# Kernel optimization log

Measured on AMD Instinct MI355X. Metric: run time of the kernel, lower is better.

The kernel has to match this reference:

```python
import jax, jax.numpy as jnp
import numpy as np

B, S, D, H = 2, 2048, 1024, 8
DK = D // H            # 128
TOPK = int(0.25 * S)   # 512, matches int(topk_ratio * attn_scores.shape[-1])


def setup_inputs() -> dict:
    root = jax.random.key(0)
    ks = jax.random.split(root, 11)
    s = 1.0 / np.sqrt(D)  # nn.Linear default init scale
    def lin(kw, kb):
        W = jax.random.uniform(kw, (D, D), jnp.float32, -s, s)
        b = jax.random.uniform(kb, (D,), jnp.float32, -s, s)
        return W, b
    Wq, bq = lin(ks[0], ks[1])
    Wk, bk = lin(ks[2], ks[3])
    Wv, bv = lin(ks[4], ks[5])
    Wo, bo = lin(ks[6], ks[7])
    return {
        "query": jax.random.normal(ks[8], (B, S, D), jnp.float32),
        "key": jax.random.normal(ks[9], (B, S, D), jnp.float32),
        "value": jax.random.normal(ks[10], (B, S, D), jnp.float32),
        "Wq": Wq, "bq": bq, "Wk": Wk, "bk": bk,
        "Wv": Wv, "bv": bv, "Wo": Wo, "bo": bo,
    }


def reference(query, key, value, Wq, bq, Wk, bk, Wv, bv, Wo, bo):
    # Projections + split heads: [B,S,D] -> [B,S,H,DK]
    Q = (query @ Wq + bq).reshape(B, S, H, DK)
    K = (key   @ Wk + bk).reshape(B, S, H, DK)
    V = (value @ Wv + bv).reshape(B, S, H, DK)

    # Full attention scores [B,H,S,S]
    scores = jnp.einsum('nqhd,nkhd->nhqk', Q, K) / np.sqrt(DK).astype(np.float32)

    # Top-k per query row, scatter into a -1e20-filled tensor
    top_val, top_idx = jax.lax.top_k(scores, TOPK)  # [B,H,S,TOPK]
    bi = jnp.arange(B)[:, None, None, None]
    hi = jnp.arange(H)[None, :, None, None]
    qi = jnp.arange(S)[None, None, :, None]
    sparse = jnp.full(scores.shape, -1e20, scores.dtype).at[bi, hi, qi, top_idx].set(top_val)

    weights = jax.nn.softmax(sparse, axis=-1)                      # [B,H,S,S]
    attn = jnp.einsum('nhql,nlhd->nqhd', weights, V).reshape(B, S, D)
    out = attn @ Wo + bo
    return out, weights
```

## Files before the change

### kernel.cpp

```cpp
#include <hip/hip_runtime.h>
#include <hip/hip_bf16.h>
#include <math.h>

namespace {

constexpr int Bb   = 2;
constexpr int Ss   = 2048;
constexpr int Dd   = 1024;
constexpr int Hh   = 8;
constexpr int DKk  = 128;
constexpr int KTOP = 512;
constexpr int BH    = Bb * Hh;
constexpr int MROWS = Bb * Ss;
constexpr float SCALE = 0.08838834764831845f;

typedef __attribute__((ext_vector_type(8))) short short8t;
typedef __attribute__((ext_vector_type(4))) short short4t;
typedef __attribute__((ext_vector_type(4))) float f32x4;

__device__ inline ushort f2bf(float x) {
  const unsigned u = __float_as_uint(x);
  return (ushort)((u + 0x7FFFu + ((u >> 16) & 1u)) >> 16);
}
__device__ inline float bf2f(ushort h) {
  return __uint_as_float(((unsigned)h) << 16);
}
struct HL { short h, l; };
__device__ inline HL split1(float x) {
  HL r;
  const ushort hu = f2bf(x);
  r.h = (short)hu;
  r.l = (short)f2bf(x - bf2f(hu));
  return r;
}

__device__ inline unsigned key_of(float v) {
  const unsigned u = __float_as_uint(v);
  return (u & 0x80000000u) ? ~u : (u | 0x80000000u);
}
__device__ inline float key_to_float(unsigned k) {
  const unsigned u = (k & 0x80000000u) ? (k & 0x7FFFFFFFu) : ~k;
  return __uint_as_float(u);
}

__device__ inline void gload16(const void* g, void* l) {
  __builtin_amdgcn_global_load_lds(
      (const __attribute__((address_space(1))) unsigned int*)g,
      (__attribute__((address_space(3))) unsigned int*)l, 16, 0, 0);
}

__global__ __launch_bounds__(256) void split_inputs(
    const float* __restrict__ query, const float* __restrict__ keyi,
    const float* __restrict__ value,
    ushort* __restrict__ qsh, ushort* __restrict__ qsl,
    ushort* __restrict__ ksh, ushort* __restrict__ ksl,
    ushort* __restrict__ vsb)
{
  const int z = blockIdx.y;
  const size_t i = ((size_t)blockIdx.x * 256 + threadIdx.x) * 8;
  const float* src = (z == 0) ? query : (z == 1) ? keyi : value;
  const float4 v0 = *(const float4*)(src + i);
  const float4 v1 = *(const float4*)(src + i + 4);
  if (z < 2) {
    ushort* oh = (z == 0) ? qsh : ksh;
    ushort* ol = (z == 0) ? qsl : ksl;
    short8t h, lo;
    HL r;
    r = split1(v0.x); h[0] = r.h; lo[0] = r.l;
    r = split1(v0.y); h[1] = r.h; lo[1] = r.l;
    r = split1(v0.z); h[2] = r.h; lo[2] = r.l;
    r = split1(v0.w); h[3] = r.h; lo[3] = r.l;
    r = split1(v1.x); h[4] = r.h; lo[4] = r.l;
    r = split1(v1.y); h[5] = r.h; lo[5] = r.l;
    r = split1(v1.z); h[6] = r.h; lo[6] = r.l;
    r = split1(v1.w); h[7] = r.h; lo[7] = r.l;
    *(short8t*)(oh + i) = h;
    *(short8t*)(ol + i) = lo;
  } else {
    short8t h;
    h[0] = (short)f2bf(v0.x); h[1] = (short)f2bf(v0.y);
    h[2] = (short)f2bf(v0.z); h[3] = (short)f2bf(v0.w);
    h[4] = (short)f2bf(v1.x); h[5] = (short)f2bf(v1.y);
    h[6] = (short)f2bf(v1.z); h[7] = (short)f2bf(v1.w);
    *(short8t*)(vsb + i) = h;
  }
}

__global__ __launch_bounds__(256) void transpose_prep(
    const float* __restrict__ Wq, const float* __restrict__ Wk,
    const float* __restrict__ Wv, const float* __restrict__ Wo,
    ushort* __restrict__ WqTh, ushort* __restrict__ WqTl,
    ushort* __restrict__ WkTh, ushort* __restrict__ WkTl,
    ushort* __restrict__ WvT,  ushort* __restrict__ WoT)
{
  __shared__ float tile[32][33];
  const int z = blockIdx.z;
  const float* W = (z == 0) ? Wq : (z == 1) ? Wk : (z == 2) ? Wv : Wo;
  const int t  = threadIdx.x;
  const int c0 = blockIdx.x * 32, r0 = blockIdx.y * 32;
  const int lr = t >> 3, lc4 = (t & 7) * 4;
  const float4 v = *(const float4*)(W + (size_t)(r0 + lr) * Dd + c0 + lc4);
  tile[lr][lc4 + 0] = v.x; tile[lr][lc4 + 1] = v.y;
  tile[lr][lc4 + 2] = v.z; tile[lr][lc4 + 3] = v.w;
  __syncthreads();
  const int oc = t >> 3, or4 = (t & 7) * 4;
  const size_t o = (size_t)(c0 + oc) * Dd + r0 + or4;
  if (z < 2) {
    ushort* Th = (z == 0) ? WqTh : WkTh;
    ushort* Tl = (z == 0) ? WqTl : WkTl;
    short4t oh, ol;
    HL r;
    r = split1(tile[or4 + 0][oc]); oh[0] = r.h; ol[0] = r.l;
    r = split1(tile[or4 + 1][oc]); oh[1] = r.h; ol[1] = r.l;
    r = split1(tile[or4 + 2][oc]); oh[2] = r.h; ol[2] = r.l;
    r = split1(tile[or4 + 3][oc]); oh[3] = r.h; ol[3] = r.l;
    *(short4t*)(Th + o) = oh;
    *(short4t*)(Tl + o) = ol;
  } else {
    ushort* Wt = (z == 2) ? WvT : WoT;
    short4t ov;
    ov[0] = (short)f2bf(tile[or4 + 0][oc]);
    ov[1] = (short)f2bf(tile[or4 + 1][oc]);
    ov[2] = (short)f2bf(tile[or4 + 2][oc]);
    ov[3] = (short)f2bf(tile[or4 + 3][oc]);
    *(short4t*)(Wt + o) = ov;
  }
}

__global__ __launch_bounds__(256) void mfma_proj(
    const ushort* __restrict__ qsh, const ushort* __restrict__ qsl,
    const ushort* __restrict__ ksh, const ushort* __restrict__ ksl,
    const ushort* __restrict__ vsb,
    const ushort* __restrict__ WqTh, const ushort* __restrict__ WqTl,
    const ushort* __restrict__ WkTh, const ushort* __restrict__ WkTl,
    const ushort* __restrict__ WvT,
    const float* __restrict__ bq, const float* __restrict__ bk,
    const float* __restrict__ bv,
    ushort* __restrict__ Qh, ushort* __restrict__ Ql,
    ushort* __restrict__ Kh, ushort* __restrict__ Kl,
    ushort* __restrict__ Vt)
{
  __shared__ ushort Ah[128 * 32];
  __shared__ ushort Al[128 * 32];
  __shared__ ushort Bh[128 * 32];
  __shared__ ushort Bl[128 * 32];
  const int t  = threadIdx.x;
  const int z  = blockIdx.z;
  const int m0 = blockIdx.x * 128;
  const int n0 = blockIdx.y * 128;
  const int l  = t & 63, wv = t >> 6;
  const int wr = wv >> 1, wc = wv & 1;
  const int lrow = l & 15, lhi = l >> 4;

  const ushort* Ah_g = (z == 0) ? qsh : (z == 1) ? ksh : vsb;
  const ushort* Al_g = (z == 0) ? qsl : (z == 1) ? ksl : nullptr;
  const ushort* Bth  = (z == 0) ? WqTh : (z == 1) ? WkTh : WvT;
  const ushort* Btl  = (z == 0) ? WqTl : (z == 1) ? WkTl : nullptr;
  const float*  bias = (z == 0) ? bq   : (z == 1) ? bk   : bv;
  const bool    splitTerms = (z < 2);

  f32x4 acc[4][4] = {};

  for (int kt = 0; kt < Dd; kt += 32) {
#pragma unroll
    for (int p = 0; p < 2; ++p) {
      const int baseRow = p * 64 + wv * 16;
      const int row  = baseRow + (l >> 2);
      const int gl   = (l & 3) ^ (row & 3);
      const size_t ao = (size_t)(m0 + row) * Dd + kt + gl * 8;
      const size_t bo = (size_t)(n0 + row) * Dd + kt + gl * 8;
      gload16(Ah_g + ao, &Ah[baseRow * 32]);
      gload16(Bth + bo, &Bh[baseRow * 32]);
      if (splitTerms) {
        gload16(Al_g + ao, &Al[baseRow * 32]);
        gload16(Btl + bo, &Bl[baseRow * 32]);
      }
    }
    __syncthreads();

    short8t ah[4], al[4], bh[4], bl[4];
#pragma unroll
    for (int i = 0; i < 4; ++i) {
      const int row = wr * 64 + i * 16 + lrow;
      const int idx = row * 32 + ((lhi ^ (row & 3)) << 3);
      ah[i] = *(const short8t*)&Ah[idx];
      if (splitTerms) al[i] = *(const short8t*)&Al[idx];
    }
#pragma unroll
    for (int j = 0; j < 4; ++j) {
      const int row = wc * 64 + j * 16 + lrow;
      const int idx = row * 32 + ((lhi ^ (row & 3)) << 3);
      bh[j] = *(const short8t*)&Bh[idx];
      if (splitTerms) bl[j] = *(const short8t*)&Bl[idx];
    }
#pragma unroll
    for (int i = 0; i < 4; ++i)
#pragma unroll
      for (int j = 0; j < 4; ++j) {
        acc[i][j] = __builtin_amdgcn_mfma_f32_16x16x32_bf16(ah[i], bh[j], acc[i][j], 0, 0, 0);
        if (splitTerms) {
          acc[i][j] = __builtin_amdgcn_mfma_f32_16x16x32_bf16(ah[i], bl[j], acc[i][j], 0, 0, 0);
          acc[i][j] = __builtin_amdgcn_mfma_f32_16x16x32_bf16(al[i], bh[j], acc[i][j], 0, 0, 0);
        }
      }
    __syncthreads();
  }

#pragma unroll
  for (int i = 0; i < 4; ++i) {
#pragma unroll
    for (int j = 0; j < 4; ++j) {
      const int nn = n0 + wc * 64 + j * 16 + lrow;
#pragma unroll
      for (int r = 0; r < 4; ++r) {
        const int mm = m0 + wr * 64 + i * 16 + lhi * 4 + r;
        const float v = acc[i][j][r] + bias[nn];
        const int bb = mm >> 11, s = mm & (Ss - 1);
        const int hh = nn >> 7,  dk = nn & (DKk - 1);
        if (z < 2) {
          const size_t o = (((size_t)(bb * Hh + hh)) * Ss + s) * DKk + dk;
          const HL rr = split1(v);
          if (z == 0) { Qh[o] = (ushort)rr.h; Ql[o] = (ushort)rr.l; }
          else        { Kh[o] = (ushort)rr.h; Kl[o] = (ushort)rr.l; }
        } else {
          Vt[((size_t)((bb * Hh + hh) * DKk + dk)) * Ss + s] = f2bf(v);
        }
      }
    }
  }
}

__global__ __launch_bounds__(256) void mfma_scores(
    const ushort* __restrict__ Qh, const ushort* __restrict__ Ql,
    const ushort* __restrict__ Kh, const ushort* __restrict__ Kl,
    unsigned* __restrict__ wtsOut)
{
  __shared__ ushort Ah[128 * 32];
  __shared__ ushort Al[128 * 32];
  __shared__ ushort Bh[128 * 32];
  __shared__ ushort Bl[128 * 32];
  const int t  = threadIdx.x;
  const int z  = blockIdx.z;
  const int n0 = blockIdx.x * 128;
  const int m0 = blockIdx.y * 128;
  const int l  = t & 63, wv = t >> 6;
  const int wr = wv >> 1, wc = wv & 1;
  const int lrow = l & 15, lhi = l >> 4;
  const size_t boff = (size_t)z * Ss * DKk;

  f32x4 acc[4][4] = {};

  for (int kt = 0; kt < DKk; kt += 32) {
#pragma unroll
    for (int p = 0; p < 2; ++p) {
      const int baseRow = p * 64 + wv * 16;
      const int row  = baseRow + (l >> 2);
      const int gl   = (l & 3) ^ (row & 3);
      const size_t ao = boff + (size_t)(m0 + row) * DKk + kt + gl * 8;
      const size_t bo = boff + (size_t)(n0 + row) * DKk + kt + gl * 8;
      gload16(Qh + ao, &Ah[baseRow * 32]);
      gload16(Ql + ao, &Al[baseRow * 32]);
      gload16(Kh + bo, &Bh[baseRow * 32]);
      gload16(Kl + bo, &Bl[baseRow * 32]);
    }
    __syncthreads();

    short8t ah[4], al[4], bh[4], bl[4];
#pragma unroll
    for (int i = 0; i < 4; ++i) {
      const int row = wr * 64 + i * 16 + lrow;
      const int idx = row * 32 + ((lhi ^ (row & 3)) << 3);
      ah[i] = *(const short8t*)&Ah[idx];
      al[i] = *(const short8t*)&Al[idx];
    }
#pragma unroll
    for (int j = 0; j < 4; ++j) {
      const int row = wc * 64 + j * 16 + lrow;
      const int idx = row * 32 + ((lhi ^ (row & 3)) << 3);
      bh[j] = *(const short8t*)&Bh[idx];
      bl[j] = *(const short8t*)&Bl[idx];
    }
#pragma unroll
    for (int i = 0; i < 4; ++i)
#pragma unroll
      for (int j = 0; j < 4; ++j) {
        acc[i][j] = __builtin_amdgcn_mfma_f32_16x16x32_bf16(ah[i], bh[j], acc[i][j], 0, 0, 0);
        acc[i][j] = __builtin_amdgcn_mfma_f32_16x16x32_bf16(ah[i], bl[j], acc[i][j], 0, 0, 0);
        acc[i][j] = __builtin_amdgcn_mfma_f32_16x16x32_bf16(al[i], bh[j], acc[i][j], 0, 0, 0);
      }
    __syncthreads();
  }

#pragma unroll
  for (int i = 0; i < 4; ++i)
#pragma unroll
    for (int j = 0; j < 4; ++j) {
      const int nn = n0 + wc * 64 + j * 16 + lrow;
#pragma unroll
      for (int r = 0; r < 4; ++r) {
        const int mm = m0 + wr * 64 + i * 16 + lhi * 4 + r;
        wtsOut[(size_t)z * Ss * Ss + (size_t)mm * Ss + nn] =
            key_of(acc[i][j][r] * SCALE);
      }
    }
}

__global__ __launch_bounds__(256) void mfma_oproj(
    const float* __restrict__ pv0, const float* __restrict__ pv1,
    const ushort* __restrict__ Bt,
    const float* __restrict__ bias, float* __restrict__ Cout)
{
  __shared__ ushort As[128 * 64];
  __shared__ ushort Bs[128 * 64];
  const int t  = threadIdx.x;
  const int m0 = blockIdx.x * 128;
  const int n0 = blockIdx.y * 128;
  const int l  = t & 63, wv = t >> 6;
  const int wr = wv >> 1, wc = wv & 1;
  const int lrow = l & 15, lhi = l >> 4;

  f32x4 acc[4][4] = {};

  for (int kt = 0; kt < Dd; kt += 64) {
#pragma unroll
    for (int p = 0; p < 4; ++p) {
      const int baseRow = p * 32 + wv * 8;
      const int brow = baseRow + (l >> 3);
      const int bgl  = (l & 7) ^ (brow & 7);
      gload16(Bt + (size_t)(n0 + brow) * Dd + kt + bgl * 8, &Bs[baseRow * 64]);
      const int li = p * 256 + t, row = li >> 3, g = li & 7;
      const int sw = row * 64 + ((g ^ (row & 7)) << 3);
      const size_t ao = (size_t)(m0 + row) * Dd + kt + g * 8;
      const float4 a0 = *(const float4*)(pv0 + ao);
      const float4 a1 = *(const float4*)(pv0 + ao + 4);
      const float4 c0 = *(const float4*)(pv1 + ao);
      const float4 c1 = *(const float4*)(pv1 + ao + 4);
      short8t sa;
      sa[0] = (short)f2bf(a0.x + c0.x); sa[1] = (short)f2bf(a0.y + c0.y);
      sa[2] = (short)f2bf(a0.z + c0.z); sa[3] = (short)f2bf(a0.w + c0.w);
      sa[4] = (short)f2bf(a1.x + c1.x); sa[5] = (short)f2bf(a1.y + c1.y);
      sa[6] = (short)f2bf(a1.z + c1.z); sa[7] = (short)f2bf(a1.w + c1.w);
      *(short8t*)&As[sw] = sa;
    }
    __syncthreads();

#pragma unroll
    for (int kk = 0; kk < 2; ++kk) {
      short8t a[4], b[4];
      const int g = kk * 4 + lhi;
#pragma unroll
      for (int i = 0; i < 4; ++i) {
        const int row = wr * 64 + i * 16 + lrow;
        a[i] = *(const short8t*)&As[row * 64 + ((g ^ (row & 7)) << 3)];
      }
#pragma unroll
      for (int j = 0; j < 4; ++j) {
        const int row = wc * 64 + j * 16 + lrow;
        b[j] = *(const short8t*)&Bs[row * 64 + ((g ^ (row & 7)) << 3)];
      }
#pragma unroll
      for (int i = 0; i < 4; ++i)
#pragma unroll
        for (int j = 0; j < 4; ++j)
          acc[i][j] = __builtin_amdgcn_mfma_f32_16x16x32_bf16(a[i], b[j], acc[i][j], 0, 0, 0);
    }
    __syncthreads();
  }

#pragma unroll
  for (int i = 0; i < 4; ++i)
#pragma unroll
    for (int j = 0; j < 4; ++j) {
      const int nn = n0 + wc * 64 + j * 16 + lrow;
#pragma unroll
      for (int r = 0; r < 4; ++r) {
        const int mm = m0 + wr * 64 + i * 16 + lhi * 4 + r;
        Cout[(size_t)mm * Dd + nn] = acc[i][j][r] + bias[nn];
      }
    }
}

__global__ __launch_bounds__(256) void pv_split(
    const float* __restrict__ Wts, const ushort* __restrict__ VtAll,
    float* __restrict__ pvp)
{
  __shared__ ushort As[128 * 64];
  __shared__ ushort Bs[128 * 64];
  const int t  = threadIdx.x;
  const int ks = blockIdx.x;
  const int m0 = blockIdx.y * 128;
  const int z  = blockIdx.z;
  const int l  = t & 63, wv = t >> 6;
  const int wr = wv >> 1, wc = wv & 1;
  const int lrow = l & 15, lhi = l >> 4;

  const float*  Af = Wts + (size_t)z * Ss * Ss;
  const ushort* Bt = VtAll + (size_t)z * DKk * Ss;

  f32x4 acc[4][4] = {};

  for (int kt = ks * 1024; kt < ks * 1024 + 1024; kt += 64) {
#pragma unroll
    for (int p = 0; p < 4; ++p) {
      const int baseRow = p * 32 + wv * 8;
      const int brow = baseRow + (l >> 3);
      const int bgl  = (l & 7) ^ (brow & 7);
      gload16(Bt + (size_t)brow * Ss + kt + bgl * 8, &Bs[baseRow * 64]);
      const int li = p * 256 + t, row = li >> 3, g = li & 7;
      const int sw = row * 64 + ((g ^ (row & 7)) << 3);
      const float* src = Af + (size_t)(m0 + row) * Ss + kt + g * 8;
      const float4 v0 = *(const float4*)src;
      const float4 v1 = *(const float4*)(src + 4);
      short8t sa;
      sa[0] = (short)f2bf(v0.x); sa[1] = (short)f2bf(v0.y);
      sa[2] = (short)f2bf(v0.z); sa[3] = (short)f2bf(v0.w);
      sa[4] = (short)f2bf(v1.x); sa[5] = (short)f2bf(v1.y);
      sa[6] = (short)f2bf(v1.z); sa[7] = (short)f2bf(v1.w);
      *(short8t*)&As[sw] = sa;
    }
    __syncthreads();

#pragma unroll
    for (int kk = 0; kk < 2; ++kk) {
      short8t a[4], b[4];
      const int g = kk * 4 + lhi;
#pragma unroll
      for (int i = 0; i < 4; ++i) {
        const int row = wr * 64 + i * 16 + lrow;
        a[i] = *(const short8t*)&As[row * 64 + ((g ^ (row & 7)) << 3)];
      }
#pragma unroll
      for (int j = 0; j < 4; ++j) {
        const int row = wc * 64 + j * 16 + lrow;
        b[j] = *(const short8t*)&Bs[row * 64 + ((g ^ (row & 7)) << 3)];
      }
#pragma unroll
      for (int i = 0; i < 4; ++i)
#pragma unroll
        for (int j = 0; j < 4; ++j)
          acc[i][j] = __builtin_amdgcn_mfma_f32_16x16x32_bf16(a[i], b[j], acc[i][j], 0, 0, 0);
    }
    __syncthreads();
  }

  const int bb = z >> 3, hh = z & 7;
  float* outp = pvp + (size_t)ks * MROWS * Dd;
#pragma unroll
  for (int i = 0; i < 4; ++i)
#pragma unroll
    for (int j = 0; j < 4; ++j) {
      const int nn = wc * 64 + j * 16 + lrow;
#pragma unroll
      for (int r = 0; r < 4; ++r) {
        const int mm = m0 + wr * 64 + i * 16 + lhi * 4 + r;
        outp[((size_t)(bb * Ss + mm)) * Dd + hh * DKk + nn] = acc[i][j][r];
      }
    }
}

__global__ __launch_bounds__(256) void topk_softmax(float* __restrict__ wts)
{
  __shared__ unsigned histAll[4][1088];

  const int lane = threadIdx.x & 63;
  const int wv   = threadIdx.x >> 6;
  const int row  = blockIdx.x * 4 + wv;
  float* rowp = wts + (size_t)row * Ss;
  unsigned* rowu = (unsigned*)rowp;
  unsigned* h = histAll[wv];

  unsigned k[32];
  unsigned lmax = 0u;
#pragma unroll
  for (int i = 0; i < 8; ++i) {
    const uint4 v = *(const uint4*)(rowu + i * 256 + lane * 4);
    k[i * 4 + 0] = v.x; k[i * 4 + 1] = v.y;
    k[i * 4 + 2] = v.z; k[i * 4 + 3] = v.w;
    lmax = max(max(lmax, max(v.x, v.y)), max(v.z, v.w));
  }
#pragma unroll
  for (int off = 32; off > 0; off >>= 1) lmax = max(lmax, __shfl_xor(lmax, off));
  const float m = key_to_float(lmax);

  unsigned needK = KTOP, tieC = 0u, prefix = 0u;
  unsigned T;

  {
#pragma unroll
    for (int i = 0; i < 17; ++i) h[lane + i * 64] = 0u;
#pragma unroll
    for (int i = 0; i < 32; ++i) {
      const unsigned b = k[i] >> 22;
      atomicAdd(&h[b + (b >> 4)], 1u);
    }
    unsigned b[16], lsum = 0u;
#pragma unroll
    for (int i = 0; i < 16; ++i) { b[i] = h[lane * 17 + i]; lsum += b[i]; }
    unsigned s = lsum;
#pragma unroll
    for (int off = 1; off < 64; off <<= 1) {
      const unsigned v = __shfl_down(s, off);
      if (lane + off < 64) s += v;
    }
    unsigned run = s - lsum;
    unsigned fb = 0u, fn = 0u, ft = 0u;
    bool found = false;
#pragma unroll
    for (int i = 15; i >= 0; --i) {
      const unsigned c = b[i];
      if (!found && c > 0u && run < needK && run + c >= needK) {
        found = true; fb = (unsigned)(lane * 16 + i); fn = needK - run; ft = c;
      }
      run += c;
    }
    const unsigned long long msk = __ballot(found);
    const int src = (int)__ffsll(msk) - 1;
    prefix = __shfl(fb, src) << 22;
    needK  = __shfl(fn, src);
    tieC   = __shfl(ft, src);
  }
  T = prefix;

  if (tieC != needK) {
#pragma unroll
    for (int pass = 0; pass < 2; ++pass) {
      const int sh = (pass == 0) ? 14 : 6;
      const int ph = sh + 8;
#pragma unroll
      for (int i = 0; i < 5; ++i) h[lane + i * 64] = 0u;
      const unsigned pcmp = prefix >> ph;
#pragma unroll
      for (int i = 0; i < 32; ++i) {
        if ((k[i] >> ph) == pcmp) {
          const unsigned b = (k[i] >> sh) & 255u;
          atomicAdd(&h[b + (b >> 4)], 1u);
        }
      }
      unsigned b4[4], lsum = 0u;
#pragma unroll
      for (int i = 0; i < 4; ++i) {
        const unsigned x = (unsigned)(lane * 4 + i);
        b4[i] = h[x + (x >> 4)];
        lsum += b4[i];
      }
      unsigned s = lsum;
#pragma unroll
      for (int off = 1; off < 64; off <<= 1) {
        const unsigned v = __shfl_down(s, off);
        if (lane + off < 64) s += v;
      }
      unsigned run = s - lsum;
      unsigned fb = 0u, fn = 0u, ft = 0u;
      bool found = false;
#pragma unroll
      for (int i = 3; i >= 0; --i) {
        const unsigned c = b4[i];
        if (!found && c > 0u && run < needK && run + c >= needK) {
          found = true; fb = (unsigned)(lane * 4 + i); fn = needK - run; ft = c;
        }
        run += c;
      }
      const unsigned long long msk = __ballot(found);
      const int src = (int)__ffsll(msk) - 1;
      prefix |= __shfl(fb, src) << sh;
      needK   = __shfl(fn, src);
      tieC    = __shfl(ft, src);
      if (tieC == needK) break;
    }
    T = prefix;

    if (tieC != needK) {
      h[lane] = 0u;
      if (lane < 4) h[64 + lane] = 0u;
      const unsigned pcmp = prefix >> 6;
#pragma unroll
      for (int i = 0; i < 32; ++i) {
        if ((k[i] >> 6) == pcmp) {
          const unsigned b = k[i] & 63u;
          atomicAdd(&h[b + (b >> 4)], 1u);
        }
      }
      const unsigned b0 = h[lane + (lane >> 4)];
      unsigned s = b0;
#pragma unroll
      for (int off = 1; off < 64; off <<= 1) {
        const unsigned v = __shfl_down(s, off);
        if (lane + off < 64) s += v;
      }
      const unsigned run = s - b0;
      const bool found = (b0 > 0u && run < needK && run + b0 >= needK);
      const unsigned long long msk = __ballot(found);
      const int src = (int)__ffsll(msk) - 1;
      T     = prefix | (unsigned)__shfl((unsigned)lane, src);
      needK = __shfl(needK - run, src);
      tieC  = __shfl(b0, src);
    }
  }

  if (tieC != needK) {
    unsigned R = 0u;
#pragma unroll
    for (int i = 0; i < 8; ++i) {
      unsigned myEq = 0u;
#pragma unroll
      for (int c = 0; c < 4; ++c) myEq += (k[i * 4 + c] == T);
      unsigned ps = myEq;
#pragma unroll
      for (int off = 1; off < 64; off <<= 1) {
        const unsigned v = __shfl_up(ps, off);
        if (lane >= off) ps += v;
      }
      unsigned before = R + ps - myEq;
#pragma unroll
      for (int c = 0; c < 4; ++c) {
        if (k[i * 4 + c] == T) {
          if (before >= needK) k[i * 4 + c] = 0u;
          ++before;
        }
      }
      R += __shfl(ps, 63);
    }
  }

  float lz = 0.f;
#pragma unroll
  for (int i = 0; i < 32; ++i) {
    const unsigned kk = k[i];
    const float w = (kk >= T) ? __expf(key_to_float(kk) - m) : 0.f;
    k[i] = __float_as_uint(w);
    lz += w;
  }
#pragma unroll
  for (int off = 32; off > 0; off >>= 1) lz += __shfl_xor(lz, off);
  const float Zi = 1.0f / lz;

#pragma unroll
  for (int i = 0; i < 8; ++i) {
    float4 o;
    o.x = __uint_as_float(k[i * 4 + 0]) * Zi;
    o.y = __uint_as_float(k[i * 4 + 1]) * Zi;
    o.z = __uint_as_float(k[i * 4 + 2]) * Zi;
    o.w = __uint_as_float(k[i * 4 + 3]) * Zi;
    *(float4*)(rowu + i * 256 + lane * 4) = o;
  }
}

}

extern "C" void kernel_launch(void* const* d_in, const int* in_sizes, int n_in,
                              void* d_out_v, int out_size, void* d_ws, size_t ws_size,
                              hipStream_t stream)
{
  const float* query = (const float*)d_in[0];
  const float* key   = (const float*)d_in[1];
  const float* value = (const float*)d_in[2];
  const float* Wq = (const float*)d_in[3];  const float* bq = (const float*)d_in[4];
  const float* Wk = (const float*)d_in[5];  const float* bk = (const float*)d_in[6];
  const float* Wv = (const float*)d_in[7];  const float* bv = (const float*)d_in[8];
  const float* Wo = (const float*)d_in[9];  const float* bo = (const float*)d_in[10];

  float* d_out = (float*)d_out_v;
  float* outp  = d_out;
  float* wts   = d_out + (size_t)Bb * Ss * Dd;

  const size_t PROJ = (size_t)MROWS * Dd;
  const size_t DD2  = (size_t)Dd * Dd;

  ushort* ws    = (ushort*)d_ws;
  ushort* Qh    = ws;
  ushort* Ql    = Qh + PROJ;
  ushort* Kh    = Ql + PROJ;
  ushort* Kl    = Kh + PROJ;
  ushort* wreg  = Kl + PROJ;
  ushort* WqTh  = wreg;
  ushort* WqTl  = wreg + DD2;
  ushort* WkTh  = wreg + 2 * DD2;
  ushort* WkTl  = wreg + 3 * DD2;
  ushort* WvT   = wreg + 4 * DD2;
  ushort* WoT   = wreg + 5 * DD2;
  ushort* Vt    = wreg + 6 * DD2;
  float*  pvp   = (float*)Qh;

  ushort* qsh = (ushort*)wts;
  ushort* qsl = qsh + PROJ;
  ushort* ksh = qsh + 2 * PROJ;
  ushort* ksl = qsh + 3 * PROJ;
  ushort* vsb = qsh + 4 * PROJ;

  const dim3 blk(256);

  transpose_prep<<<dim3(32, 32, 4), blk, 0, stream>>>(
      Wq, Wk, Wv, Wo, WqTh, WqTl, WkTh, WkTl, WvT, WoT);

  split_inputs<<<dim3((int)(PROJ / 2048), 3), blk, 0, stream>>>(
      query, key, value, qsh, qsl, ksh, ksl, vsb);

  mfma_proj<<<dim3(MROWS / 128, Dd / 128, 3), blk, 0, stream>>>(
      qsh, qsl, ksh, ksl, vsb, WqTh, WqTl, WkTh, WkTl, WvT,
      bq, bk, bv, Qh, Ql, Kh, Kl, Vt);

  mfma_scores<<<dim3(Ss / 128, Ss / 128, BH), blk, 0, stream>>>(
      Qh, Ql, Kh, Kl, (unsigned*)wts);

  topk_softmax<<<dim3(BH * Ss / 4), blk, 0, stream>>>(wts);

  pv_split<<<dim3(2, Ss / 128, BH), blk, 0, stream>>>(wts, Vt, pvp);

  mfma_oproj<<<dim3(MROWS / 128, Dd / 128), blk, 0, stream>>>(
      pvp, pvp + (size_t)MROWS * Dd, WoT, bo, outp);
}
```

Before: 367.4 us.

## Replace split-K PV with direct full-K PV writing bf16 attention output

The PV matmul no longer splits K into two halves with fp32 partial outputs. Each block now covers 64 query rows over the full sequence length and writes the attention output directly as bf16. The output projection then loads that bf16 input with async 16-byte global-to-LDS loads instead of reading two fp32 partials, summing them and converting. This removes the partial-sum round trip and the conversion work, but halves the M tile, so the same grid size gets a smaller per-block tile and a longer K loop.

```diff
diff --git a/kernel.cpp b/kernel.cpp
--- a/kernel.cpp
+++ b/kernel.cpp
@@ -306,8 +306,7 @@
 }
 
 __global__ __launch_bounds__(256) void mfma_oproj(
-    const float* __restrict__ pv0, const float* __restrict__ pv1,
-    const ushort* __restrict__ Bt,
+    const ushort* __restrict__ Ab, const ushort* __restrict__ Bt,
     const float* __restrict__ bias, float* __restrict__ Cout)
 {
   __shared__ ushort As[128 * 64];
@@ -325,22 +324,10 @@
 #pragma unroll
     for (int p = 0; p < 4; ++p) {
       const int baseRow = p * 32 + wv * 8;
-      const int brow = baseRow + (l >> 3);
-      const int bgl  = (l & 7) ^ (brow & 7);
-      gload16(Bt + (size_t)(n0 + brow) * Dd + kt + bgl * 8, &Bs[baseRow * 64]);
-      const int li = p * 256 + t, row = li >> 3, g = li & 7;
-      const int sw = row * 64 + ((g ^ (row & 7)) << 3);
-      const size_t ao = (size_t)(m0 + row) * Dd + kt + g * 8;
-      const float4 a0 = *(const float4*)(pv0 + ao);
-      const float4 a1 = *(const float4*)(pv0 + ao + 4);
-      const float4 c0 = *(const float4*)(pv1 + ao);
-      const float4 c1 = *(const float4*)(pv1 + ao + 4);
-      short8t sa;
-      sa[0] = (short)f2bf(a0.x + c0.x); sa[1] = (short)f2bf(a0.y + c0.y);
-      sa[2] = (short)f2bf(a0.z + c0.z); sa[3] = (short)f2bf(a0.w + c0.w);
-      sa[4] = (short)f2bf(a1.x + c1.x); sa[5] = (short)f2bf(a1.y + c1.y);
-      sa[6] = (short)f2bf(a1.z + c1.z); sa[7] = (short)f2bf(a1.w + c1.w);
-      *(short8t*)&As[sw] = sa;
+      const int row = baseRow + (l >> 3);
+      const int gl  = (l & 7) ^ (row & 7);
+      gload16(Ab + (size_t)(m0 + row) * Dd + kt + gl * 8, &As[baseRow * 64]);
+      gload16(Bt + (size_t)(n0 + row) * Dd + kt + gl * 8, &Bs[baseRow * 64]);
     }
     __syncthreads();
 
@@ -380,16 +367,15 @@
     }
 }
 
-__global__ __launch_bounds__(256) void pv_split(
+__global__ __launch_bounds__(256) void pv_direct(
     const float* __restrict__ Wts, const ushort* __restrict__ VtAll,
-    float* __restrict__ pvp)
-{
-  __shared__ ushort As[128 * 64];
+    ushort* __restrict__ attnb)
+{
+  __shared__ ushort As[64 * 64];
   __shared__ ushort Bs[128 * 64];
   const int t  = threadIdx.x;
-  const int ks = blockIdx.x;
-  const int m0 = blockIdx.y * 128;
-  const int z  = blockIdx.z;
+  const int m0 = blockIdx.x * 64;
+  const int z  = blockIdx.y;
   const int l  = t & 63, wv = t >> 6;
   const int wr = wv >> 1, wc = wv & 1;
   const int lrow = l & 15, lhi = l >> 4;
@@ -397,15 +383,11 @@
   const float*  Af = Wts + (size_t)z * Ss * Ss;
   const ushort* Bt = VtAll + (size_t)z * DKk * Ss;
 
-  f32x4 acc[4][4] = {};
-
-  for (int kt = ks * 1024; kt < ks * 1024 + 1024; kt += 64) {
-#pragma unroll
-    for (int p = 0; p < 4; ++p) {
-      const int baseRow = p * 32 + wv * 8;
-      const int brow = baseRow + (l >> 3);
-      const int bgl  = (l & 7) ^ (brow & 7);
-      gload16(Bt + (size_t)brow * Ss + kt + bgl * 8, &Bs[baseRow * 64]);
+  f32x4 acc[2][4] = {};
+
+  for (int kt = 0; kt < Ss; kt += 64) {
+#pragma unroll
+    for (int p = 0; p < 2; ++p) {
       const int li = p * 256 + t, row = li >> 3, g = li & 7;
       const int sw = row * 64 + ((g ^ (row & 7)) << 3);
       const float* src = Af + (size_t)(m0 + row) * Ss + kt + g * 8;
@@ -418,15 +400,22 @@
       sa[6] = (short)f2bf(v1.z); sa[7] = (short)f2bf(v1.w);
       *(short8t*)&As[sw] = sa;
     }
+#pragma unroll
+    for (int p = 0; p < 4; ++p) {
+      const int baseRow = p * 32 + wv * 8;
+      const int brow = baseRow + (l >> 3);
+      const int bgl  = (l & 7) ^ (brow & 7);
+      gload16(Bt + (size_t)brow * Ss + kt + bgl * 8, &Bs[baseRow * 64]);
+    }
     __syncthreads();
 
 #pragma unroll
     for (int kk = 0; kk < 2; ++kk) {
-      short8t a[4], b[4];
+      short8t a[2], b[4];
       const int g = kk * 4 + lhi;
 #pragma unroll
-      for (int i = 0; i < 4; ++i) {
-        const int row = wr * 64 + i * 16 + lrow;
+      for (int i = 0; i < 2; ++i) {
+        const int row = wr * 32 + i * 16 + lrow;
         a[i] = *(const short8t*)&As[row * 64 + ((g ^ (row & 7)) << 3)];
       }
 #pragma unroll
@@ -435,7 +424,7 @@
         b[j] = *(const short8t*)&Bs[row * 64 + ((g ^ (row & 7)) << 3)];
       }
 #pragma unroll
-      for (int i = 0; i < 4; ++i)
+      for (int i = 0; i < 2; ++i)
 #pragma unroll
         for (int j = 0; j < 4; ++j)
           acc[i][j] = __builtin_amdgcn_mfma_f32_16x16x32_bf16(a[i], b[j], acc[i][j], 0, 0, 0);
@@ -444,16 +433,15 @@
   }
 
   const int bb = z >> 3, hh = z & 7;
-  float* outp = pvp + (size_t)ks * MROWS * Dd;
-#pragma unroll
-  for (int i = 0; i < 4; ++i)
+#pragma unroll
+  for (int i = 0; i < 2; ++i)
 #pragma unroll
     for (int j = 0; j < 4; ++j) {
       const int nn = wc * 64 + j * 16 + lrow;
 #pragma unroll
       for (int r = 0; r < 4; ++r) {
-        const int mm = m0 + wr * 64 + i * 16 + lhi * 4 + r;
-        outp[((size_t)(bb * Ss + mm)) * Dd + hh * DKk + nn] = acc[i][j][r];
+        const int mm = m0 + wr * 32 + i * 16 + lhi * 4 + r;
+        attnb[((size_t)(bb * Ss + mm)) * Dd + hh * DKk + nn] = f2bf(acc[i][j][r]);
       }
     }
 }
@@ -679,7 +667,7 @@
   ushort* WvT   = wreg + 4 * DD2;
   ushort* WoT   = wreg + 5 * DD2;
   ushort* Vt    = wreg + 6 * DD2;
-  float*  pvp   = (float*)Qh;
+  ushort* attnb = Qh;
 
   ushort* qsh = (ushort*)wts;
   ushort* qsl = qsh + PROJ;
@@ -704,8 +692,8 @@
 
   topk_softmax<<<dim3(BH * Ss / 4), blk, 0, stream>>>(wts);
 
-  pv_split<<<dim3(2, Ss / 128, BH), blk, 0, stream>>>(wts, Vt, pvp);
+  pv_direct<<<dim3(Ss / 64, BH), blk, 0, stream>>>(wts, Vt, attnb);
 
   mfma_oproj<<<dim3(MROWS / 128, Dd / 128), blk, 0, stream>>>(
-      pvp, pvp + (size_t)MROWS * Dd, WoT, bo, outp);
-}
+      attnb, WoT, bo, outp);
+}
```

Result: no change. 363.3 us (-1.1%).
